# Kernel optimization log

Hardware: AMD Instinct MI355X
Metric: run time of the kernel (lower is better)

## Reference

```python
import jax, jax.numpy as jnp
import numpy as np

COS_BASIS_NO = 13
COS_SHIFT = 1.0
COS_SCALE = 3.0


def make_cos_basis(T_no):
    # [13, T_no] raised-cosine basis in log-time, matching the torch loop
    i = jnp.arange(COS_BASIS_NO, dtype=jnp.float32)[:, None]
    phi = 0.5 * jnp.pi * i
    x = jnp.arange(T_no, dtype=jnp.float32)[None, :]
    raw = COS_SCALE * jnp.log(x + COS_SHIFT)
    basis = 0.5 * jnp.cos(raw - phi) + 0.5
    mask = (raw >= phi - jnp.pi) & (raw <= phi + jnp.pi)
    return jnp.where(mask, basis, jnp.float32(0.0))


def causal_conv(x, kern):
    # x: [T, S], kern: [S, K] (unflipped, kern[:,0] = weight on x[t-1]).
    # Matches torch: pad K zeros in front, depthwise conv with flipped kernel, drop last.
    T, S = x.shape
    K = kern.shape[1]
    xp = jnp.pad(x, ((K, 0), (0, 0)))            # [T+K, S]
    lhs = xp.T[None]                              # [1, S, T+K]
    rhs = kern[:, None, ::-1]                     # [S, 1, K]
    out = jax.lax.conv_general_dilated(
        lhs, rhs, window_strides=(1,), padding='VALID',
        dimension_numbers=('NCW', 'OIW', 'NCW'), feature_group_count=S)
    return out[0].T[:-1]                          # [T, S]


def setup_inputs() -> dict:
    T_data, T_no, sub_no, E_no, I_no = 500000, 200, 20, 200, 50
    key = jax.random.key(0)
    ks = jax.random.split(key, 8)
    S_e = (jax.random.uniform(ks[0], (T_data, E_no)) < 0.05).astype(jnp.float32)
    S_i = (jax.random.uniform(ks[1], (T_data, I_no)) < 0.05).astype(jnp.float32)
    Z = (jax.random.uniform(ks[2], (T_data, sub_no)) < 0.10).astype(jnp.float32)
    C_syn_e = jax.nn.one_hot(jax.random.randint(ks[3], (E_no,), 0, sub_no), sub_no).T.astype(jnp.float32)
    C_syn_i = jax.nn.one_hot(jax.random.randint(ks[4], (I_no,), 0, sub_no), sub_no).T.astype(jnp.float32)
    C_den = (jax.random.uniform(ks[5], (sub_no, sub_no)) < 0.1).astype(jnp.float32)
    Tau_syn = jnp.ones((sub_no, 2), jnp.float32)
    Delta_syn = jnp.zeros((sub_no, 2), jnp.float32)
    W_syn = jnp.full((sub_no, 2), 0.01, jnp.float32)
    W_spk = jax.random.normal(ks[6], (sub_no, COS_BASIS_NO), jnp.float32) * 0.01
    W_hist = jax.random.normal(ks[7], (sub_no, COS_BASIS_NO), jnp.float32) * 0.1
    Theta = jnp.full((sub_no,), -5.0, jnp.float32)
    return dict(S_e=S_e, S_i=S_i, Z=Z, C_den=C_den, C_syn_e=C_syn_e, C_syn_i=C_syn_i,
                Tau_syn=Tau_syn, Delta_syn=Delta_syn, W_syn=W_syn, W_spk=W_spk,
                W_hist=W_hist, Theta=Theta, T_no=T_no)


def reference(S_e, S_i, Z, C_den, C_syn_e, C_syn_i, Tau_syn, Delta_syn, W_syn, W_spk, W_hist, Theta, T_no):
    # --- spike_convolve ---
    syn_e = S_e @ C_syn_e.T                       # [T, sub_no]
    syn_i = S_i @ C_syn_i.T
    t = jnp.arange(T_no, dtype=jnp.float32)[None, :]
    t_e = jnp.maximum(t - Delta_syn[:, 0:1], 0.0)
    t_i = jnp.maximum(t - Delta_syn[:, 1:2], 0.0)
    t_tau_e = t_e / Tau_syn[:, 0:1] ** 2
    t_tau_i = t_i / Tau_syn[:, 1:2] ** 2
    e_kern = t_tau_e * jnp.exp(-t_tau_e) * W_syn[:, 0:1] ** 2   # [sub_no, T_no]
    i_kern = -(t_tau_i * jnp.exp(-t_tau_i) * W_syn[:, 1:2] ** 2)
    syn = causal_conv(syn_e, e_kern) + causal_conv(syn_i, i_kern)
    # --- train_forward ---
    cos_basis = make_cos_basis(T_no)              # [13, T_no]
    spk_kern = W_spk @ cos_basis                  # [sub_no, T_no]
    hist_kern = W_hist @ cos_basis
    spk_filt = causal_conv(Z, spk_kern) @ C_den.T
    hist_filt = causal_conv(Z, hist_kern)
    P = jax.nn.sigmoid(syn + Theta[None, :] + hist_filt + spk_filt)
    out_filters = jnp.vstack((e_kern, i_kern, spk_kern, hist_kern))  # [4*sub_no, T_no]
    return P, out_filters
```

## Files before the change

kernel.cpp:

```cpp
#include <hip/hip_runtime.h>
#include <hip/hip_bf16.h>
#include <math.h>

typedef unsigned int u32;
typedef unsigned short u16;
typedef __bf16 bf16x8 __attribute__((ext_vector_type(8)));
typedef float f32x4 __attribute__((ext_vector_type(4)));
typedef u32 u32x4 __attribute__((ext_vector_type(4)));
typedef u32 u32x2 __attribute__((ext_vector_type(2)));

#define T_DATA 500000
#define KNO    200
#define SUB    20
#define E_NO   200
#define I_NO   50
#define NBAS   13
#define PI_F   3.14159265358979f
#define KKN    7
#define P_SZ   (T_DATA*SUB)
#define MT_TOT (T_DATA/16)
#define TCH    256
#define NCHUNKS_TOT ((T_DATA + TCH - 1)/TCH)
#define GBLK   ((MT_TOT + 3)/4)
#define WSTR   472

__device__ __forceinline__ float bf2f(u16 v){
  union { u32 u; float f; } x; x.u = ((u32)v) << 16; return x.f;
}
__device__ __forceinline__ u16 f2bf(float f){
  union { float f; u32 u; } x; x.f = f;
  u32 u = x.u;
  return (u16)((u + 0x7FFFu + ((u >> 16) & 1u)) >> 16);
}
__device__ __forceinline__ u16 trunc_bf(float f){
  union { float f; u32 u; } x; x.f = f;
  return (u16)(x.u >> 16);
}
__device__ __forceinline__ u32 f2u(float f){
  union { float f; u32 u; } x; x.f = f; return x.u;
}

__device__ __forceinline__ float filt_val(int type, int s, int j,
    const float* Tau, const float* Del, const float* Wsyn,
    const float* Wspk, const float* Whist){
  if (type < 2){
    float tau = Tau[s*2+type];
    float del = Del[s*2+type];
    float w   = Wsyn[s*2+type];
    float t   = fmaxf((float)j - del, 0.0f);
    float tt  = t / (tau*tau);
    float v   = tt * expf(-tt) * (w*w);
    return (type == 1) ? -v : v;
  } else {
    const float* W = (type == 2) ? Wspk : Whist;
    float raw = 3.0f * logf((float)j + 1.0f);
    float acc = 0.0f;
#pragma unroll
    for (int b = 0; b < NBAS; b++){
      float d = raw - 0.5f*PI_F*(float)b;
      float bas = (d >= -PI_F && d <= PI_F) ? (0.5f*cosf(d) + 0.5f) : 0.0f;
      acc += W[s*NBAS + b] * bas;
    }
    return acc;
  }
}

__global__ void k_setup(const float* Tau, const float* Del, const float* Wsyn,
                        const float* Wspk, const float* Whist,
                        const float* Ce, const float* Ci,
                        float* out, u16* afrag, u16* bfrag){
  int bid = blockIdx.x;
  int tid = threadIdx.x;
  if (bid < 80){
    int r = bid, type = r / SUB, s = r % SUB;
    for (int j = tid; j < KNO; j += 64)
      out[P_SZ + r*KNO + j] = filt_val(type, s, j, Tau, Del, Wsyn, Wspk, Whist);
  } else if (bid < 80 + 4*SUB*KKN){
    int b = bid - 80;
    int kk = b % KKN;
    int ts = b / KKN;
    int type = ts / SUB, s = ts % SUB;
    __shared__ float kf[KNO];
    for (int j = tid; j < KNO; j += 64)
      kf[j] = filt_val(type, s, j, Tau, Del, Wsyn, Wspk, Whist);
    __syncthreads();
    int l = tid;
    int m = l & 15, kg = l >> 4;
    int off = 200 - 32*kk;
    u32 p[4];
#pragma unroll
    for (int h = 0; h < 4; h++){
      int u0 = kg*8 + 2*h;
      int i0 = off + m - 1 - u0;
      int i1 = i0 - 1;
      u16 lo = (i0 >= 0 && i0 < KNO) ? f2bf(kf[i0]) : (u16)0;
      u16 hi = (i1 >= 0 && i1 < KNO) ? f2bf(kf[i1]) : (u16)0;
      p[h] = (u32)lo | ((u32)hi << 16);
    }
    u32* dst = (u32*)(afrag + (size_t)b*512 + l*8);
    dst[0]=p[0]; dst[1]=p[1]; dst[2]=p[2]; dst[3]=p[3];
  } else {
    const int NE = 2*7*512, NI = 2*2*512, NZ = 2*1*512;
    int b = bid - (80 + 4*SUB*KKN);
    for (int x = b*64 + tid; x < NE+NI+NZ; x += 40*64){
      int src, base, KT;
      if (x < NE){ src=0; base=x;       KT=7; }
      else if (x < NE+NI){ src=1; base=x-NE;    KT=2; }
      else {               src=2; base=x-NE-NI; KT=1; }
      int nt = base / (KT*512);
      int rem = base % (KT*512);
      int kt = rem / 512;
      int le = rem % 512;
      int l = le / 8, e = le % 8;
      int n = nt*16 + (l & 15);
      int k = kt*32 + (l >> 4)*8 + e;
      u16 v = 0;
      if (src == 0){ if (n < SUB && k < E_NO) v = trunc_bf(Ce[n*E_NO + k]); }
      else if (src == 1){ if (n < SUB && k < I_NO) v = trunc_bf(Ci[n*I_NO + k]); }
      else { if (n < SUB && k == n) v = trunc_bf(1.0f); }
      bfrag[x] = v;
    }
  }
}

template<int W, int KT>
__device__ __forceinline__ void gather_body(int bid, const float* __restrict__ src,
                                            const u16* __restrict__ bfrag,
                                            u16* __restrict__ dst){
  int wv = threadIdx.x >> 6, lane = threadIdx.x & 63;
  int mt = bid*4 + wv;
  if (mt >= MT_TOT) return;
  int t0 = mt*16;
  int m = lane & 15, kg = lane >> 4;
  const size_t NW = (size_t)T_DATA * W;

  u32 wb[KT][8];
#pragma unroll
  for (int kt = 0; kt < KT; kt++){
    bool skip;
    if (W == 200)      skip = (kt == 6) && (kg > 0);
    else if (W == 50)  skip = (kt == 1) && (kg == 3);
    else               skip = (kg == 3);
    size_t cs = (size_t)(t0 + m)*W + kt*32 + kg*8;
    if (skip){
#pragma unroll
      for (int e = 0; e < 8; e++) wb[kt][e] = 0u;
    } else if (cs + 8 <= NW){
      if (W == 50){
        *(u32x2*)&wb[kt][0] = *(const u32x2*)(src + cs);
        *(u32x2*)&wb[kt][2] = *(const u32x2*)(src + cs + 2);
        *(u32x2*)&wb[kt][4] = *(const u32x2*)(src + cs + 4);
        *(u32x2*)&wb[kt][6] = *(const u32x2*)(src + cs + 6);
      } else {
        *(u32x4*)&wb[kt][0] = *(const u32x4*)(src + cs);
        *(u32x4*)&wb[kt][4] = *(const u32x4*)(src + cs + 4);
      }
    } else {
#pragma unroll
      for (int e = 0; e < 8; e++){
        size_t idx = cs + e;
        wb[kt][e] = (idx < NW) ? f2u(src[idx]) : 0u;
      }
    }
  }

  f32x4 acc0 = {0.f,0.f,0.f,0.f}, acc1 = {0.f,0.f,0.f,0.f};
#pragma unroll
  for (int kt = 0; kt < KT; kt++){
    union { bf16x8 v; u16 h[8]; } au;
#pragma unroll
    for (int e = 0; e < 8; e++) au.h[e] = (u16)(wb[kt][e] >> 16);
    bf16x8 b0 = *(const bf16x8*)(bfrag + kt*512 + lane*8);
    bf16x8 b1 = *(const bf16x8*)(bfrag + (KT + kt)*512 + lane*8);
    acc0 = __builtin_amdgcn_mfma_f32_16x16x32_bf16(au.v, b0, acc0, 0, 0, 0);
    acc1 = __builtin_amdgcn_mfma_f32_16x16x32_bf16(au.v, b1, acc1, 0, 0, 0);
  }
  int i0 = kg*4;
  {
    u32 lo = (u32)f2bf(acc0[0]) | ((u32)f2bf(acc0[1]) << 16);
    u32 hi = (u32)f2bf(acc0[2]) | ((u32)f2bf(acc0[3]) << 16);
    u32* d = (u32*)(dst + (size_t)m*T_DATA + t0 + i0);
    d[0] = lo; d[1] = hi;
  }
  if (m < SUB - 16){
    u32 lo = (u32)f2bf(acc1[0]) | ((u32)f2bf(acc1[1]) << 16);
    u32 hi = (u32)f2bf(acc1[2]) | ((u32)f2bf(acc1[3]) << 16);
    u32* d = (u32*)(dst + (size_t)(16 + m)*T_DATA + t0 + i0);
    d[0] = lo; d[1] = hi;
  }
}

__global__ __launch_bounds__(256, 4) void k_gather_all(
    const float* __restrict__ S_e, const float* __restrict__ S_i,
    const float* __restrict__ Z, const u16* __restrict__ bfrag,
    u16* __restrict__ xe, u16* __restrict__ xi, u16* __restrict__ zt){
  int bid = blockIdx.x;
  if (bid < GBLK)            gather_body<200,7>(bid,          S_e, bfrag,                       xe);
  else if (bid < 2*GBLK)     gather_body<50, 2>(bid - GBLK,   S_i, bfrag + 2*7*512,             xi);
  else                       gather_body<20, 1>(bid - 2*GBLK, Z,   bfrag + 2*7*512 + 2*2*512,   zt);
}

__global__ __launch_bounds__(512, 2) void k_conv2(
    const u16* __restrict__ xe, const u16* __restrict__ xi,
    const u16* __restrict__ zt, const u16* __restrict__ afrag,
    const float* __restrict__ Cden, const float* __restrict__ Theta,
    float* __restrict__ out)
{
  __shared__ __align__(16) u16 win[3*SUB*WSTR];
  __shared__ float lcden[SUB*SUB];
  __shared__ float lth[SUB];

  int tid = threadIdx.x;
  for (int i = tid; i < SUB*SUB; i += 512) lcden[i] = Cden[i];
  if (tid < SUB) lth[tid] = Theta[tid];

  int bid = blockIdx.x;
  int xcd = bid & 7, sb = bid >> 3;
  const int q8 = NCHUNKS_TOT >> 3, r8 = NCHUNKS_TOT & 7;
  int c = (xcd < r8 ? xcd*(q8+1) : r8*(q8+1) + (xcd-r8)*q8) + sb;

  int wv = tid >> 6, lane = tid & 63;
  int m = lane & 15, kg = lane >> 4;
  long t0w = (long)c*TCH - 200;

  for (int i = tid; i < 3*SUB*58; i += 512){
    int arr = i / (SUB*58);
    int rem = i - arr*(SUB*58);
    int ch  = rem / 58;
    int i8  = rem - ch*58;
    long g0 = t0w + i8*8;
    const u16* gp = (arr == 0 ? xe : (arr == 1 ? xi : zt)) + (size_t)ch*T_DATA;
    u16* lp = win + (size_t)(arr*SUB + ch)*WSTR + i8*8;
    if (g0 >= 0 && g0 + 8 <= T_DATA){
      *(bf16x8*)lp = *(const bf16x8*)(gp + g0);
    } else {
#pragma unroll
      for (int e = 0; e < 8; e++){
        long g = g0 + e;
        lp[e] = (g >= 0 && g < T_DATA) ? gp[g] : (u16)0;
      }
    }
  }
  __syncthreads();

  int boffB = 16*m + 8*kg;
  int toff  = 16*m + 4*kg;
  f32x4 A0[5], A1[5];
  if (wv < 4){
    int ch0 = wv*5;
#pragma unroll
    for (int q = 0; q < 5; q++){
      int ch = ch0 + q;
      const u16* be = win + (size_t)(0*SUB + ch)*WSTR + boffB;
      const u16* bi = win + (size_t)(1*SUB + ch)*WSTR + boffB;
      const u16* ae = afrag + (size_t)((0*SUB + ch)*KKN)*512 + lane*8;
      const u16* ai = afrag + (size_t)((1*SUB + ch)*KKN)*512 + lane*8;
      f32x4 a = {0.f,0.f,0.f,0.f};
#pragma unroll
      for (int kk = 0; kk < KKN; kk++){
        a = __builtin_amdgcn_mfma_f32_16x16x32_bf16(
              *(const bf16x8*)(ae + kk*512), *(const bf16x8*)(be + 32*kk), a, 0,0,0);
        a = __builtin_amdgcn_mfma_f32_16x16x32_bf16(
              *(const bf16x8*)(ai + kk*512), *(const bf16x8*)(bi + 32*kk), a, 0,0,0);
      }
      A0[q] = a;
    }
  } else {
    int ch0 = (wv - 4)*5;
#pragma unroll
    for (int q = 0; q < 5; q++){
      int ch = ch0 + q;
      const u16* bz = win + (size_t)(2*SUB + ch)*WSTR + boffB;
      const u16* a2 = afrag + (size_t)((2*SUB + ch)*KKN)*512 + lane*8;
      const u16* a3 = afrag + (size_t)((3*SUB + ch)*KKN)*512 + lane*8;
      f32x4 s = {0.f,0.f,0.f,0.f}, h = {0.f,0.f,0.f,0.f};
#pragma unroll
      for (int kk = 0; kk < KKN; kk++){
        bf16x8 b = *(const bf16x8*)(bz + 32*kk);
        s = __builtin_amdgcn_mfma_f32_16x16x32_bf16(*(const bf16x8*)(a2 + kk*512), b, s, 0,0,0);
        h = __builtin_amdgcn_mfma_f32_16x16x32_bf16(*(const bf16x8*)(a3 + kk*512), b, h, 0,0,0);
      }
      A0[q] = s; A1[q] = h;
    }
  }
  __syncthreads();

  u16* rr = win;
  if (wv < 4){
#pragma unroll
    for (int q = 0; q < 5; q++){
      int ch = wv*5 + q;
      u32* d = (u32*)(rr + ch*TCH + toff);
      d[0] = (u32)f2bf(A0[q][0]) | ((u32)f2bf(A0[q][1]) << 16);
      d[1] = (u32)f2bf(A0[q][2]) | ((u32)f2bf(A0[q][3]) << 16);
    }
  } else {
#pragma unroll
    for (int q = 0; q < 5; q++){
      int ch = (wv - 4)*5 + q;
      u32* d1 = (u32*)(rr + (SUB + ch)*TCH + toff);
      d1[0] = (u32)f2bf(A0[q][0]) | ((u32)f2bf(A0[q][1]) << 16);
      d1[1] = (u32)f2bf(A0[q][2]) | ((u32)f2bf(A0[q][3]) << 16);
      u32* d2 = (u32*)(rr + (2*SUB + ch)*TCH + toff);
      d2[0] = (u32)f2bf(A1[q][0]) | ((u32)f2bf(A1[q][1]) << 16);
      d2[1] = (u32)f2bf(A1[q][2]) | ((u32)f2bf(A1[q][3]) << 16);
    }
  }
  __syncthreads();

  float* pbuf = (float*)win;
  int t = tid >> 1, h = tid & 1;
  float spkv[SUB];
#pragma unroll
  for (int s = 0; s < SUB; s++) spkv[s] = bf2f(rr[(SUB + s)*TCH + t]);
  float res[10];
#pragma unroll
  for (int j = 0; j < 10; j++){
    int sp = h*10 + j;
    float msum = bf2f(rr[sp*TCH + t]) + lth[sp] + bf2f(rr[(2*SUB + sp)*TCH + t]);
#pragma unroll
    for (int s = 0; s < SUB; s++) msum += lcden[sp*SUB + s] * spkv[s];
    res[j] = 1.0f/(1.0f + expf(-msum));
  }
  __syncthreads();
#pragma unroll
  for (int j = 0; j < 10; j++) pbuf[t*21 + h*10 + j] = res[j];
  __syncthreads();

  int t0c = c*TCH;
  int tv = min(TCH, T_DATA - t0c);
  int np4 = tv*SUB/4;
  for (int i = tid; i < np4; i += 512){
    int p = i*4;
    int tt = p/20, sp = p - tt*20;
    float4 v;
    v.x = pbuf[tt*21 + sp];   v.y = pbuf[tt*21 + sp+1];
    v.z = pbuf[tt*21 + sp+2]; v.w = pbuf[tt*21 + sp+3];
    *(float4*)(out + (size_t)t0c*SUB + p) = v;
  }
}

extern "C" void kernel_launch(void* const* d_in, const int* in_sizes, int n_in,
                              void* d_out, int out_size, void* d_ws, size_t ws_size,
                              hipStream_t stream){
  const float* S_e  = (const float*)d_in[0];
  const float* S_i  = (const float*)d_in[1];
  const float* Z    = (const float*)d_in[2];
  const float* Cden = (const float*)d_in[3];
  const float* C_e  = (const float*)d_in[4];
  const float* C_i  = (const float*)d_in[5];
  const float* Tau  = (const float*)d_in[6];
  const float* Del  = (const float*)d_in[7];
  const float* Wsyn = (const float*)d_in[8];
  const float* Wspk = (const float*)d_in[9];
  const float* Whist= (const float*)d_in[10];
  const float* Theta= (const float*)d_in[11];
  float* out = (float*)d_out;

  u16* xe    = (u16*)d_ws;
  u16* xi    = xe + (size_t)SUB*T_DATA;
  u16* zt    = xi + (size_t)SUB*T_DATA;
  u16* afrag = zt + (size_t)SUB*T_DATA;
  u16* bfrag = afrag + (size_t)4*SUB*KKN*512;
  size_t need = ((size_t)3*SUB*T_DATA + (size_t)4*SUB*KKN*512 + 10240) * 2;
  if (ws_size < need) return;

  k_setup<<<80 + 4*SUB*KKN + 40, 64, 0, stream>>>(
      Tau, Del, Wsyn, Wspk, Whist, C_e, C_i, out, afrag, bfrag);

  k_gather_all<<<3*GBLK, 256, 0, stream>>>(S_e, S_i, Z, bfrag, xe, xi, zt);

  k_conv2<<<NCHUNKS_TOT, 512, 0, stream>>>(xe, xi, zt, afrag, Cden, Theta, out);
}
```

Before: 212.6 us.

## Stage gather input tiles into LDS via direct global-to-LDS loads

The gather kernel now copies each wave's contiguous 16-row input tile into shared memory with global_load_lds (16-byte and 4-byte variants), then reads MFMA A-fragments from LDS instead of issuing strided per-lane global loads. This aims to make global reads fully coalesced and to cut VGPR pressure from buffering the whole tile in registers. It adds about 53KB of LDS per block and a block-wide barrier, and lowers the launch-bounds occupancy hint from 4 to 3 blocks per CU.

```diff
diff --git a/kernel.cpp b/kernel.cpp
--- a/kernel.cpp
+++ b/kernel.cpp
@@ -23,6 +23,17 @@
 #define NCHUNKS_TOT ((T_DATA + TCH - 1)/TCH)
 #define GBLK   ((MT_TOT + 3)/4)
 #define WSTR   472
+#define SWU    3328
+
+typedef __attribute__((address_space(1))) const u32 gas_u32;
+typedef __attribute__((address_space(3))) u32 las_u32;
+
+__device__ __forceinline__ void gll16(const void* g, u32* l){
+  __builtin_amdgcn_global_load_lds((gas_u32*)g, (las_u32*)l, 16, 0, 0);
+}
+__device__ __forceinline__ void gll4(const void* g, u32* l){
+  __builtin_amdgcn_global_load_lds((gas_u32*)g, (las_u32*)l, 4, 0, 0);
+}
 
 __device__ __forceinline__ float bf2f(u16 v){
   union { u32 u; float f; } x; x.u = ((u32)v) << 16; return x.f;
@@ -35,9 +46,6 @@
 __device__ __forceinline__ u16 trunc_bf(float f){
   union { float f; u32 u; } x; x.f = f;
   return (u16)(x.u >> 16);
-}
-__device__ __forceinline__ u32 f2u(float f){
-  union { float f; u32 u; } x; x.f = f; return x.u;
 }
 
 __device__ __forceinline__ float filt_val(int type, int s, int j,
@@ -124,52 +132,76 @@
 }
 
 template<int W, int KT>
-__device__ __forceinline__ void gather_body(int bid, const float* __restrict__ src,
-                                            const u16* __restrict__ bfrag,
-                                            u16* __restrict__ dst){
+__device__ __forceinline__ void gather_body2(int bid, const float* __restrict__ src,
+                                             const u16* __restrict__ bfrag,
+                                             u16* __restrict__ dst, u32* sw){
   int wv = threadIdx.x >> 6, lane = threadIdx.x & 63;
   int mt = bid*4 + wv;
-  if (mt >= MT_TOT) return;
+  bool act = (mt < MT_TOT);
+  int m = lane & 15, kg = lane >> 4;
+
+  if (act){
+    const char* gb = (const char*)src + (size_t)mt*(16*W*4);
+    const char* gend16 = (const char*)src + (size_t)T_DATA*W*4 - 16;
+    if (W == 200){
+#pragma unroll
+      for (int j = 0; j < 13; j++){
+        const char* g = gb + j*1024 + lane*16;
+        if (g > gend16) g = gend16;
+        gll16(g, sw + j*256);
+      }
+    } else if (W == 50){
+#pragma unroll
+      for (int j = 0; j < 3; j++){
+        const char* g = gb + j*1024 + lane*16;
+        if (g > gend16) g = gend16;
+        gll16(g, sw + j*256);
+      }
+      {
+        const char* g = gb + 3072 + lane*4;
+        const char* gend4 = (const char*)src + (size_t)T_DATA*W*4 - 4;
+        if (g > gend4) g = gend4;
+        gll4(g, sw + 768);
+      }
+    } else {
+#pragma unroll
+      for (int j = 0; j < 2; j++){
+        const char* g = gb + j*1024 + lane*16;
+        if (g > gend16) g = gend16;
+        gll16(g, sw + j*256);
+      }
+    }
+  }
+  __syncthreads();
+
+  if (!act) return;
   int t0 = mt*16;
-  int m = lane & 15, kg = lane >> 4;
-  const size_t NW = (size_t)T_DATA * W;
-
-  u32 wb[KT][8];
+  f32x4 acc0 = {0.f,0.f,0.f,0.f}, acc1 = {0.f,0.f,0.f,0.f};
 #pragma unroll
   for (int kt = 0; kt < KT; kt++){
     bool skip;
     if (W == 200)      skip = (kt == 6) && (kg > 0);
     else if (W == 50)  skip = (kt == 1) && (kg == 3);
     else               skip = (kg == 3);
-    size_t cs = (size_t)(t0 + m)*W + kt*32 + kg*8;
+    union { bf16x8 v; u16 h[8]; } au;
     if (skip){
 #pragma unroll
-      for (int e = 0; e < 8; e++) wb[kt][e] = 0u;
-    } else if (cs + 8 <= NW){
-      if (W == 50){
-        *(u32x2*)&wb[kt][0] = *(const u32x2*)(src + cs);
-        *(u32x2*)&wb[kt][2] = *(const u32x2*)(src + cs + 2);
-        *(u32x2*)&wb[kt][4] = *(const u32x2*)(src + cs + 4);
-        *(u32x2*)&wb[kt][6] = *(const u32x2*)(src + cs + 6);
+      for (int e = 0; e < 8; e++) au.h[e] = 0;
+    } else {
+      int fo = m*W + kt*32 + kg*8;
+      u32 wb[8];
+      if (W == 200){
+        *(u32x4*)&wb[0] = *(const u32x4*)(sw + fo);
+        *(u32x4*)&wb[4] = *(const u32x4*)(sw + fo + 4);
       } else {
-        *(u32x4*)&wb[kt][0] = *(const u32x4*)(src + cs);
-        *(u32x4*)&wb[kt][4] = *(const u32x4*)(src + cs + 4);
-      }
-    } else {
-#pragma unroll
-      for (int e = 0; e < 8; e++){
-        size_t idx = cs + e;
-        wb[kt][e] = (idx < NW) ? f2u(src[idx]) : 0u;
-      }
-    }
-  }
-
-  f32x4 acc0 = {0.f,0.f,0.f,0.f}, acc1 = {0.f,0.f,0.f,0.f};
-#pragma unroll
-  for (int kt = 0; kt < KT; kt++){
-    union { bf16x8 v; u16 h[8]; } au;
-#pragma unroll
-    for (int e = 0; e < 8; e++) au.h[e] = (u16)(wb[kt][e] >> 16);
+        *(u32x2*)&wb[0] = *(const u32x2*)(sw + fo);
+        *(u32x2*)&wb[2] = *(const u32x2*)(sw + fo + 2);
+        *(u32x2*)&wb[4] = *(const u32x2*)(sw + fo + 4);
+        *(u32x2*)&wb[6] = *(const u32x2*)(sw + fo + 6);
+      }
+#pragma unroll
+      for (int e = 0; e < 8; e++) au.h[e] = (u16)(wb[e] >> 16);
+    }
     bf16x8 b0 = *(const bf16x8*)(bfrag + kt*512 + lane*8);
     bf16x8 b1 = *(const bf16x8*)(bfrag + (KT + kt)*512 + lane*8);
     acc0 = __builtin_amdgcn_mfma_f32_16x16x32_bf16(au.v, b0, acc0, 0, 0, 0);
@@ -190,14 +222,16 @@
   }
 }
 
-__global__ __launch_bounds__(256, 4) void k_gather_all(
+__global__ __launch_bounds__(256, 3) void k_gather_all(
     const float* __restrict__ S_e, const float* __restrict__ S_i,
     const float* __restrict__ Z, const u16* __restrict__ bfrag,
     u16* __restrict__ xe, u16* __restrict__ xi, u16* __restrict__ zt){
+  __shared__ __align__(16) u32 sbuf[4*SWU];
+  u32* sw = sbuf + (threadIdx.x >> 6)*SWU;
   int bid = blockIdx.x;
-  if (bid < GBLK)            gather_body<200,7>(bid,          S_e, bfrag,                       xe);
-  else if (bid < 2*GBLK)     gather_body<50, 2>(bid - GBLK,   S_i, bfrag + 2*7*512,             xi);
-  else                       gather_body<20, 1>(bid - 2*GBLK, Z,   bfrag + 2*7*512 + 2*2*512,   zt);
+  if (bid < GBLK)            gather_body2<200,7>(bid,          S_e, bfrag,                     xe, sw);
+  else if (bid < 2*GBLK)     gather_body2<50, 2>(bid - GBLK,   S_i, bfrag + 2*7*512,           xi, sw);
+  else                       gather_body2<20, 1>(bid - 2*GBLK, Z,   bfrag + 2*7*512 + 2*2*512, zt, sw);
 }
 
 __global__ __launch_bounds__(512, 2) void k_conv2(
```

Result: faster. 207.2 us (median of 2 runs) (-2.5%).
